# Kernel tuning notes

Measured on AMD Instinct MI355X. Metric: run time of the kernel, lower is better.

Reference implementation:

```python
import jax, jax.numpy as jnp
import numpy as np

N_NODES = 100000
N_EDGES = 600000
D_IN = 128
D_HID = 128


def gcn_conv(x, W, b, src, dst, n_nodes):
    # PyG GCNConv: add self-loops, symmetric deg^-1/2 normalization,
    # linear transform, scatter-add aggregation, bias.
    xw = x @ W  # [N, H]
    self_loop = jnp.arange(n_nodes, dtype=src.dtype)
    s = jnp.concatenate([src, self_loop])  # sources j
    d = jnp.concatenate([dst, self_loop])  # targets i
    deg = jax.ops.segment_sum(jnp.ones_like(d, dtype=xw.dtype), d,
                              num_segments=n_nodes)
    dinv = jnp.where(deg > 0, jax.lax.rsqrt(deg), 0.0)
    norm = dinv[s] * dinv[d]  # [E+N]
    msg = xw[s] * norm[:, None]  # gather + scale
    out = jax.ops.segment_sum(msg, d, num_segments=n_nodes)
    return out + b


def setup_inputs() -> dict:
    key = jax.random.key(0)
    ks = jax.random.split(key, 4)
    x = jax.random.normal(ks[0], (N_NODES, D_IN), dtype=jnp.float32)
    edge_index = jax.random.randint(ks[1], (2, N_EDGES), 0, N_NODES,
                                    dtype=jnp.int32)
    W1 = jax.random.normal(ks[2], (D_IN, D_HID), dtype=jnp.float32) / np.sqrt(D_IN)
    b1 = jnp.zeros((D_HID,), dtype=jnp.float32)
    W2 = jax.random.normal(ks[3], (D_HID, D_HID), dtype=jnp.float32) / np.sqrt(D_HID)
    b2 = jnp.zeros((D_HID,), dtype=jnp.float32)
    return {"x": x, "edge_index": edge_index, "W1": W1, "b1": b1,
            "W2": W2, "b2": b2}


def reference(x, edge_index, W1, b1, W2, b2):
    src, dst = edge_index[0], edge_index[1]
    n = x.shape[0]
    z = gcn_conv(x, W1, b1, src, dst, n)
    z = jax.nn.relu(z)
    z = gcn_conv(z, W2, b2, src, dst, n)
    # decode: per-edge dot product of endpoint embeddings
    return jnp.sum(z[src] * z[dst], axis=1)  # [E]
```

## Files before the change

### kernel.cpp

```cpp
#include <hip/hip_runtime.h>


typedef __attribute__((ext_vector_type(8))) short short8;
typedef __attribute__((ext_vector_type(4))) float f32x4;

__device__ __forceinline__ unsigned bf16_rne(float x) {
  unsigned u = __builtin_bit_cast(unsigned, x);
  return (u + 0x7FFFu + ((u >> 16) & 1u)) >> 16;
}
__device__ __forceinline__ float bf2f(unsigned short u) {
  return __builtin_bit_cast(float, ((unsigned)u) << 16);
}

__device__ __forceinline__ void wpack_body(const float* __restrict__ W,
                                           short* __restrict__ Wp, int t) {
  int lane = t & 63;
  int kf = (t >> 6) & 3;
  int ct = t >> 8;
  int col = ct * 16 + (lane & 15);
  int k0 = kf * 32 + (lane >> 4) * 8;
  short* dh = Wp + ((((0 * 8 + ct) * 4 + kf) * 64) + lane) * 8;
  short* dl = Wp + ((((1 * 8 + ct) * 4 + kf) * 64) + lane) * 8;
  for (int j = 0; j < 8; ++j) {
    float w = W[(k0 + j) * 128 + col];
    unsigned h = bf16_rne(w);
    float hf = __builtin_bit_cast(float, h << 16);
    unsigned lo = bf16_rne(w - hf);
    dh[j] = (short)h;
    dl[j] = (short)lo;
  }
}

__global__ __launch_bounds__(256) void prep_kernel(const float* __restrict__ W1,
                                                   short* __restrict__ Wp1,
                                                   const float* __restrict__ W2,
                                                   short* __restrict__ Wp2,
                                                   const int* __restrict__ dst,
                                                   int* __restrict__ deg,
                                                   int* __restrict__ slot, int E) {
  const int b = blockIdx.x;
  if (b < 8) {
    wpack_body(W1, Wp1, b * 256 + threadIdx.x);
  } else if (b < 16) {
    wpack_body(W2, Wp2, (b - 8) * 256 + threadIdx.x);
  } else {
    int base = (b - 16) * 1024 + threadIdx.x;
#pragma unroll
    for (int i = 0; i < 4; ++i) {
      int e = base + i * 256;
      if (e < E) slot[e] = atomicAdd(&deg[dst[e]], 1);
    }
  }
}

__global__ __launch_bounds__(512) void scan1_kernel(const int* __restrict__ in,
                                                    int* __restrict__ tmp,
                                                    int* __restrict__ bsums, int n) {
  __shared__ int sm[2][512];
  int t = threadIdx.x;
  int gid = blockIdx.x * 512 + t;
  int v = (gid < n) ? in[gid] : 0;
  int pp = 0;
  sm[0][t] = v;
  __syncthreads();
  for (int off = 1; off < 512; off <<= 1) {
    int nv = sm[pp][t];
    if (t >= off) nv += sm[pp][t - off];
    sm[pp ^ 1][t] = nv;
    pp ^= 1;
    __syncthreads();
  }
  int inc = sm[pp][t];
  if (gid < n) tmp[gid] = inc;
  if (t == 511) bsums[blockIdx.x] = inc;
}

__global__ __launch_bounds__(256) void scan23_kernel(const int* __restrict__ tmp,
                                                     const int* __restrict__ bsums,
                                                     const int* __restrict__ deg,
                                                     int* __restrict__ rowptr,
                                                     float* __restrict__ dinv,
                                                     int n, int nb) {
  __shared__ int sm[2][256];
  __shared__ int orig[256];
  int t = threadIdx.x;
  int v = (t < nb) ? bsums[t] : 0;
  orig[t] = v;
  int pp = 0;
  sm[0][t] = v;
  __syncthreads();
  for (int off = 1; off < 256; off <<= 1) {
    int nv = sm[pp][t];
    if (t >= off) nv += sm[pp][t - off];
    sm[pp ^ 1][t] = nv;
    pp ^= 1;
    __syncthreads();
  }
  int gid = blockIdx.x * 256 + t;
  if (gid < n) {
    int b = gid >> 9;
    rowptr[gid + 1] = tmp[gid] + (sm[pp][b] - orig[b]);
    dinv[gid] = rsqrtf((float)(deg[gid] + 1));
  }
  if (gid == 0) rowptr[0] = 0;
}

__global__ __launch_bounds__(256, 4) void scatgemm_kernel(
    const int* __restrict__ src, const int* __restrict__ dst,
    const int* __restrict__ rowptr, const int* __restrict__ slot,
    int2* __restrict__ csr, int E, int SCB, const float* __restrict__ A,
    const short* __restrict__ Wp, const float* __restrict__ dinv,
    unsigned short* __restrict__ out, int M) {
  __shared__ short8 lds_a[256];

  if ((int)blockIdx.x < SCB) {
    int base = blockIdx.x * 1024 + threadIdx.x;
#pragma unroll
    for (int i = 0; i < 4; ++i) {
      int e = base + i * 256;
      if (e < E) {
        int d = dst[e];
        csr[rowptr[d] + slot[e]] = make_int2(src[e], e);
      }
    }
    return;
  }

  const int bid = blockIdx.x - SCB;
  const int tid = threadIdx.x;
  const int wave = tid >> 6;
  const int lane = tid & 63;
  const int quad = lane >> 4;
  const int l15 = lane & 15;
  const int ct0 = wave * 2;
  const int ct1 = wave * 2 + 1;
  const int colbase = wave * 32 + l15;
  const int rb0 = bid * 16;
  const bool full = (rb0 + 16 <= M);
  const short8* Wp8 = (const short8*)Wp;

  {
    const int row = tid >> 4;
    const int seg = tid & 15;
    float4 a0 = {0.f, 0.f, 0.f, 0.f}, a1 = {0.f, 0.f, 0.f, 0.f};
    if (full || rb0 + row < M) {
      const float4* p = (const float4*)A + (size_t)(rb0 + row) * 32 + seg * 2;
      a0 = p[0];
      a1 = p[1];
    }
    const float av[8] = {a0.x, a0.y, a0.z, a0.w, a1.x, a1.y, a1.z, a1.w};
    short8 w;
#pragma unroll
    for (int j = 0; j < 8; ++j) w[j] = (short)bf16_rne(av[j]);
    lds_a[row * 16 + (seg ^ (row & 7))] = w;
  }

  short8 bh0[4], bh1[4], bl0[4], bl1[4];
#pragma unroll
  for (int f = 0; f < 4; ++f) {
    bh0[f] = Wp8[((0 * 8 + ct0) * 4 + f) * 64 + lane];
    bh1[f] = Wp8[((0 * 8 + ct1) * 4 + f) * 64 + lane];
    bl0[f] = Wp8[((1 * 8 + ct0) * 4 + f) * 64 + lane];
    bl1[f] = Wp8[((1 * 8 + ct1) * 4 + f) * 64 + lane];
  }

  __syncthreads();

  short8 af[4];
#pragma unroll
  for (int f = 0; f < 4; ++f) af[f] = lds_a[l15 * 16 + ((f * 4 + quad) ^ (l15 & 7))];

  f32x4 a0h = {0.f, 0.f, 0.f, 0.f};
  f32x4 a0l = {0.f, 0.f, 0.f, 0.f};
  f32x4 a1h = {0.f, 0.f, 0.f, 0.f};
  f32x4 a1l = {0.f, 0.f, 0.f, 0.f};
#pragma unroll
  for (int f = 0; f < 4; ++f) {
    a0h = __builtin_amdgcn_mfma_f32_16x16x32_bf16(af[f], bh0[f], a0h, 0, 0, 0);
    a1h = __builtin_amdgcn_mfma_f32_16x16x32_bf16(af[f], bh1[f], a1h, 0, 0, 0);
    a0l = __builtin_amdgcn_mfma_f32_16x16x32_bf16(af[f], bl0[f], a0l, 0, 0, 0);
    a1l = __builtin_amdgcn_mfma_f32_16x16x32_bf16(af[f], bl1[f], a1l, 0, 0, 0);
  }

  if (full) {
    const f32x4 dv = *(const f32x4*)(dinv + rb0 + quad * 4);
#pragma unroll
    for (int i = 0; i < 4; ++i) {
      const int r = rb0 + quad * 4 + i;
      out[(size_t)r * 128 + colbase] =
          (unsigned short)bf16_rne((a0h[i] + a0l[i]) * dv[i]);
      out[(size_t)r * 128 + colbase + 16] =
          (unsigned short)bf16_rne((a1h[i] + a1l[i]) * dv[i]);
    }
  } else {
#pragma unroll
    for (int i = 0; i < 4; ++i) {
      const int r = rb0 + quad * 4 + i;
      if (r < M) {
        const float d = dinv[r];
        out[(size_t)r * 128 + colbase] =
            (unsigned short)bf16_rne((a0h[i] + a0l[i]) * d);
        out[(size_t)r * 128 + colbase + 16] =
            (unsigned short)bf16_rne((a1h[i] + a1l[i]) * d);
      }
    }
  }
}

__global__ __launch_bounds__(256) void agg_gemm_kernel(
    const unsigned short* __restrict__ xw, const float* __restrict__ dinv,
    const int* __restrict__ rowptr, const int2* __restrict__ csr,
    const float* __restrict__ bias, const short* __restrict__ Wp,
    unsigned short* __restrict__ out, int N) {
  __shared__ short8 z1t[16][16];

  const int tid = threadIdx.x;
  const int node0 = blockIdx.x * 16;
  const int n = tid >> 4;
  const int l = tid & 15;
  const int node = node0 + n;

  short8 o = {0, 0, 0, 0, 0, 0, 0, 0};
  if (node < N) {
    const short8* xw8 = (const short8*)xw;
    short8 sv = xw8[(size_t)node * 16 + l];
    float acc[8];
#pragma unroll
    for (int j = 0; j < 8; ++j) acc[j] = bf2f((unsigned short)sv[j]);
    int s = rowptr[node], e = rowptr[node + 1];
    int k = s;
    for (; k + 4 <= e; k += 4) {
      int j0 = csr[k].x, j1 = csr[k + 1].x, j2 = csr[k + 2].x, j3 = csr[k + 3].x;
      short8 v0 = xw8[(size_t)j0 * 16 + l];
      short8 v1 = xw8[(size_t)j1 * 16 + l];
      short8 v2 = xw8[(size_t)j2 * 16 + l];
      short8 v3 = xw8[(size_t)j3 * 16 + l];
#pragma unroll
      for (int j = 0; j < 8; ++j) {
        acc[j] += (bf2f((unsigned short)v0[j]) + bf2f((unsigned short)v1[j])) +
                  (bf2f((unsigned short)v2[j]) + bf2f((unsigned short)v3[j]));
      }
    }
    for (; k < e; ++k) {
      short8 v = xw8[(size_t)csr[k].x * 16 + l];
#pragma unroll
      for (int j = 0; j < 8; ++j) acc[j] += bf2f((unsigned short)v[j]);
    }
    float di = dinv[node];
    const float4* b4 = (const float4*)bias;
    float4 bb0 = b4[l * 2], bb1 = b4[l * 2 + 1];
    float bv[8] = {bb0.x, bb0.y, bb0.z, bb0.w, bb1.x, bb1.y, bb1.z, bb1.w};
#pragma unroll
    for (int j = 0; j < 8; ++j) {
      float v = fmaf(di, acc[j], bv[j]);
      v = fmaxf(v, 0.f);
      o[j] = (short)bf16_rne(v);
    }
  }
  z1t[n][l ^ n] = o;
  __syncthreads();

  const int wave = tid >> 6;
  const int lane = tid & 63;
  const int quad = lane >> 4;
  const int l15 = lane & 15;
  const int ct0 = wave * 2;
  const int ct1 = wave * 2 + 1;

  short8 af[4];
#pragma unroll
  for (int f = 0; f < 4; ++f) af[f] = z1t[l15][(f * 4 + quad) ^ l15];

  const short8* Wp8 = (const short8*)Wp;
  f32x4 a0h = {0.f, 0.f, 0.f, 0.f};
  f32x4 a0l = {0.f, 0.f, 0.f, 0.f};
  f32x4 a1h = {0.f, 0.f, 0.f, 0.f};
  f32x4 a1l = {0.f, 0.f, 0.f, 0.f};
#pragma unroll
  for (int f = 0; f < 4; ++f) {
    const short8 bh0 = Wp8[((0 * 8 + ct0) * 4 + f) * 64 + lane];
    const short8 bh1 = Wp8[((0 * 8 + ct1) * 4 + f) * 64 + lane];
    const short8 bl0 = Wp8[((1 * 8 + ct0) * 4 + f) * 64 + lane];
    const short8 bl1 = Wp8[((1 * 8 + ct1) * 4 + f) * 64 + lane];
    a0h = __builtin_amdgcn_mfma_f32_16x16x32_bf16(af[f], bh0, a0h, 0, 0, 0);
    a1h = __builtin_amdgcn_mfma_f32_16x16x32_bf16(af[f], bh1, a1h, 0, 0, 0);
    a0l = __builtin_amdgcn_mfma_f32_16x16x32_bf16(af[f], bl0, a0l, 0, 0, 0);
    a1l = __builtin_amdgcn_mfma_f32_16x16x32_bf16(af[f], bl1, a1l, 0, 0, 0);
  }

  if (node0 + 16 <= N) {
    const f32x4 dv = *(const f32x4*)(dinv + node0 + quad * 4);
#pragma unroll
    for (int i = 0; i < 4; ++i) {
      const int r = node0 + quad * 4 + i;
      out[(size_t)r * 128 + ct0 * 16 + l15] =
          (unsigned short)bf16_rne((a0h[i] + a0l[i]) * dv[i]);
      out[(size_t)r * 128 + ct1 * 16 + l15] =
          (unsigned short)bf16_rne((a1h[i] + a1l[i]) * dv[i]);
    }
  } else {
#pragma unroll
    for (int i = 0; i < 4; ++i) {
      const int r = node0 + quad * 4 + i;
      if (r < N) {
        const float d = dinv[r];
        out[(size_t)r * 128 + ct0 * 16 + l15] =
            (unsigned short)bf16_rne((a0h[i] + a0l[i]) * d);
        out[(size_t)r * 128 + ct1 * 16 + l15] =
            (unsigned short)bf16_rne((a1h[i] + a1l[i]) * d);
      }
    }
  }
}

__global__ __launch_bounds__(128) void agg_kernel(const unsigned short* __restrict__ xw,
                                                  const float* __restrict__ dinv,
                                                  const int* __restrict__ rowptr,
                                                  const int2* __restrict__ csr,
                                                  const float* __restrict__ bias,
                                                  unsigned short* __restrict__ out,
                                                  int relu, int N) {
  int node = blockIdx.x * 8 + (threadIdx.x >> 4);
  int l = threadIdx.x & 15;
  if (node >= N) return;
  const short8* xw8 = (const short8*)xw;
  short8 sv = xw8[(size_t)node * 16 + l];
  float acc[8];
#pragma unroll
  for (int j = 0; j < 8; ++j) acc[j] = bf2f((unsigned short)sv[j]);
  int s = rowptr[node], e = rowptr[node + 1];
  int k = s;
  for (; k + 4 <= e; k += 4) {
    int j0 = csr[k].x, j1 = csr[k + 1].x, j2 = csr[k + 2].x, j3 = csr[k + 3].x;
    short8 v0 = xw8[(size_t)j0 * 16 + l];
    short8 v1 = xw8[(size_t)j1 * 16 + l];
    short8 v2 = xw8[(size_t)j2 * 16 + l];
    short8 v3 = xw8[(size_t)j3 * 16 + l];
#pragma unroll
    for (int j = 0; j < 8; ++j) {
      acc[j] += (bf2f((unsigned short)v0[j]) + bf2f((unsigned short)v1[j])) +
                (bf2f((unsigned short)v2[j]) + bf2f((unsigned short)v3[j]));
    }
  }
  for (; k < e; ++k) {
    short8 v = xw8[(size_t)csr[k].x * 16 + l];
#pragma unroll
    for (int j = 0; j < 8; ++j) acc[j] += bf2f((unsigned short)v[j]);
  }
  float di = dinv[node];
  const float4* b4 = (const float4*)bias;
  float4 bb0 = b4[l * 2], bb1 = b4[l * 2 + 1];
  float bv[8] = {bb0.x, bb0.y, bb0.z, bb0.w, bb1.x, bb1.y, bb1.z, bb1.w};
  short8 o;
#pragma unroll
  for (int j = 0; j < 8; ++j) {
    float v = fmaf(di, acc[j], bv[j]);
    if (relu) v = fmaxf(v, 0.f);
    o[j] = (short)bf16_rne(v);
  }
  ((short8*)out)[(size_t)node * 16 + l] = o;
}

__global__ __launch_bounds__(128) void decode_kernel(const unsigned short* __restrict__ z,
                                                     const int* __restrict__ rowptr,
                                                     const int2* __restrict__ csr,
                                                     float* __restrict__ out, int N) {
  int node = blockIdx.x * 8 + (threadIdx.x >> 4);
  int l = threadIdx.x & 15;
  if (node >= N) return;
  const short8* z8 = (const short8*)z;
  short8 zv = z8[(size_t)node * 16 + l];
  float zd[8];
#pragma unroll
  for (int j = 0; j < 8; ++j) zd[j] = bf2f((unsigned short)zv[j]);
  int s = rowptr[node], e = rowptr[node + 1];
  int k = s;
  for (; k + 4 <= e; k += 4) {
    int2 c0 = csr[k], c1 = csr[k + 1], c2 = csr[k + 2], c3 = csr[k + 3];
    short8 v0 = z8[(size_t)c0.x * 16 + l];
    short8 v1 = z8[(size_t)c1.x * 16 + l];
    short8 v2 = z8[(size_t)c2.x * 16 + l];
    short8 v3 = z8[(size_t)c3.x * 16 + l];
    float p0 = 0.f, p1 = 0.f, p2 = 0.f, p3 = 0.f;
#pragma unroll
    for (int j = 0; j < 8; ++j) {
      p0 = fmaf(zd[j], bf2f((unsigned short)v0[j]), p0);
      p1 = fmaf(zd[j], bf2f((unsigned short)v1[j]), p1);
      p2 = fmaf(zd[j], bf2f((unsigned short)v2[j]), p2);
      p3 = fmaf(zd[j], bf2f((unsigned short)v3[j]), p3);
    }
#pragma unroll
    for (int off = 8; off > 0; off >>= 1) {
      p0 += __shfl_xor(p0, off);
      p1 += __shfl_xor(p1, off);
      p2 += __shfl_xor(p2, off);
      p3 += __shfl_xor(p3, off);
    }
    if (l == 0) {
      out[c0.y] = p0;
      out[c1.y] = p1;
      out[c2.y] = p2;
      out[c3.y] = p3;
    }
  }
  for (; k < e; ++k) {
    int2 c = csr[k];
    short8 v = z8[(size_t)c.x * 16 + l];
    float p = 0.f;
#pragma unroll
    for (int j = 0; j < 8; ++j) p = fmaf(zd[j], bf2f((unsigned short)v[j]), p);
#pragma unroll
    for (int off = 8; off > 0; off >>= 1) p += __shfl_xor(p, off);
    if (l == 0) out[c.y] = p;
  }
}

extern "C" void kernel_launch(void* const* d_in, const int* in_sizes, int n_in,
                              void* d_out, int out_size, void* d_ws, size_t ws_size,
                              hipStream_t stream) {
  const float* x  = (const float*)d_in[0];
  const int*   ei = (const int*)d_in[1];
  const float* W1 = (const float*)d_in[2];
  const float* b1 = (const float*)d_in[3];
  const float* W2 = (const float*)d_in[4];
  const float* b2 = (const float*)d_in[5];

  const int N = in_sizes[0] / 128;
  const int E = in_sizes[1] / 2;
  const int* src = ei;
  const int* dst = ei + E;

  char* ws = (char*)d_ws;
  size_t off = 0;
  auto alloc = [&](size_t bytes) -> void* {
    void* p = ws + off;
    off += (bytes + 255) & ~(size_t)255;
    return p;
  };
  unsigned short* bufA = (unsigned short*)alloc((size_t)N * 128 * 2);
  unsigned short* bufB = (unsigned short*)alloc((size_t)N * 128 * 2);
  float* dinv    = (float*)alloc((size_t)N * 4);
  int*   rowptr  = (int*)alloc((size_t)(N + 1) * 4);
  int2*  csr     = (int2*)alloc((size_t)E * 8);
  short* Wp1     = (short*)alloc((size_t)2 * 8 * 4 * 64 * 8 * 2);
  short* Wp2     = (short*)alloc((size_t)2 * 8 * 4 * 64 * 8 * 2);
  int*   tmp     = (int*)alloc((size_t)N * 4);
  int*   slot    = (int*)alloc((size_t)E * 4);
  int*   deg     = (int*)alloc((size_t)N * 4);
  int*   bsums   = (int*)alloc(1024);
  size_t zbytes = ((char*)bsums + 1024) - (char*)deg;
  hipMemsetAsync(deg, 0, zbytes, stream);

  const int E4B = (E + 1023) / 1024;
  const int NB = (N + 255) / 256;
  const int SB = (N + 511) / 512;
  const int G16 = (N + 15) / 16;
  const int AB16 = (N + 15) / 16;
  const int AB8 = (N + 7) / 8;

  prep_kernel<<<16 + E4B, 256, 0, stream>>>(W1, Wp1, W2, Wp2, dst, deg, slot, E);
  scan1_kernel<<<SB, 512, 0, stream>>>(deg, tmp, bsums, N);
  scan23_kernel<<<NB, 256, 0, stream>>>(tmp, bsums, deg, rowptr, dinv, N, SB);
  scatgemm_kernel<<<E4B + G16, 256, 0, stream>>>(src, dst, rowptr, slot, csr, E,
                                                 E4B, x, Wp1, dinv, bufA, N);
  agg_gemm_kernel<<<AB16, 256, 0, stream>>>(bufA, dinv, rowptr, csr, b1, Wp2,
                                            bufB, N);
  agg_kernel<<<AB8, 128, 0, stream>>>(bufB, dinv, rowptr, csr, b2, bufA, 0, N);
  decode_kernel<<<AB8, 128, 0, stream>>>(bufA, rowptr, csr, (float*)d_out, N);
}
```

Before: 259.6 us.

## Prefetch next CSR index batch in gather loops and shrink agg/decode blocks

Software-pipelines the neighbor loops in agg_gemm, agg and decode so the next four CSR entries load while the current four feature rows are gathered, hiding index-load latency. It also halves the agg and decode block size to 64 threads (one wavefront, 4 nodes per block), and doubles the edges per block in the degree-counting part of prep. The prefetch costs extra registers and may lower occupancy, and smaller blocks mean more blocks to schedule.

```diff
diff --git a/kernel.cpp b/kernel.cpp
--- a/kernel.cpp
+++ b/kernel.cpp
@@ -44,9 +44,9 @@
   } else if (b < 16) {
     wpack_body(W2, Wp2, (b - 8) * 256 + threadIdx.x);
   } else {
-    int base = (b - 16) * 1024 + threadIdx.x;
-#pragma unroll
-    for (int i = 0; i < 4; ++i) {
+    int base = (b - 16) * 2048 + threadIdx.x;
+#pragma unroll
+    for (int i = 0; i < 8; ++i) {
       int e = base + i * 256;
       if (e < E) slot[e] = atomicAdd(&deg[dst[e]], 1);
     }
@@ -229,17 +229,24 @@
     for (int j = 0; j < 8; ++j) acc[j] = bf2f((unsigned short)sv[j]);
     int s = rowptr[node], e = rowptr[node + 1];
     int k = s;
-    for (; k + 4 <= e; k += 4) {
-      int j0 = csr[k].x, j1 = csr[k + 1].x, j2 = csr[k + 2].x, j3 = csr[k + 3].x;
-      short8 v0 = xw8[(size_t)j0 * 16 + l];
-      short8 v1 = xw8[(size_t)j1 * 16 + l];
-      short8 v2 = xw8[(size_t)j2 * 16 + l];
-      short8 v3 = xw8[(size_t)j3 * 16 + l];
+    int2 c0 = {0, 0}, c1 = {0, 0}, c2 = {0, 0}, c3 = {0, 0};
+    bool have = (k + 4 <= e);
+    if (have) { c0 = csr[k]; c1 = csr[k + 1]; c2 = csr[k + 2]; c3 = csr[k + 3]; }
+    while (have) {
+      const int kn = k + 4;
+      const bool hn = (kn + 4 <= e);
+      int2 n0 = {0, 0}, n1 = {0, 0}, n2 = {0, 0}, n3 = {0, 0};
+      if (hn) { n0 = csr[kn]; n1 = csr[kn + 1]; n2 = csr[kn + 2]; n3 = csr[kn + 3]; }
+      short8 v0 = xw8[(size_t)c0.x * 16 + l];
+      short8 v1 = xw8[(size_t)c1.x * 16 + l];
+      short8 v2 = xw8[(size_t)c2.x * 16 + l];
+      short8 v3 = xw8[(size_t)c3.x * 16 + l];
 #pragma unroll
       for (int j = 0; j < 8; ++j) {
         acc[j] += (bf2f((unsigned short)v0[j]) + bf2f((unsigned short)v1[j])) +
                   (bf2f((unsigned short)v2[j]) + bf2f((unsigned short)v3[j]));
       }
+      k = kn; have = hn; c0 = n0; c1 = n1; c2 = n2; c3 = n3;
     }
     for (; k < e; ++k) {
       short8 v = xw8[(size_t)csr[k].x * 16 + l];
@@ -313,14 +320,14 @@
   }
 }
 
-__global__ __launch_bounds__(128) void agg_kernel(const unsigned short* __restrict__ xw,
-                                                  const float* __restrict__ dinv,
-                                                  const int* __restrict__ rowptr,
-                                                  const int2* __restrict__ csr,
-                                                  const float* __restrict__ bias,
-                                                  unsigned short* __restrict__ out,
-                                                  int relu, int N) {
-  int node = blockIdx.x * 8 + (threadIdx.x >> 4);
+__global__ __launch_bounds__(64) void agg_kernel(const unsigned short* __restrict__ xw,
+                                                 const float* __restrict__ dinv,
+                                                 const int* __restrict__ rowptr,
+                                                 const int2* __restrict__ csr,
+                                                 const float* __restrict__ bias,
+                                                 unsigned short* __restrict__ out,
+                                                 int relu, int N) {
+  int node = blockIdx.x * 4 + (threadIdx.x >> 4);
   int l = threadIdx.x & 15;
   if (node >= N) return;
   const short8* xw8 = (const short8*)xw;
@@ -330,17 +337,24 @@
   for (int j = 0; j < 8; ++j) acc[j] = bf2f((unsigned short)sv[j]);
   int s = rowptr[node], e = rowptr[node + 1];
   int k = s;
-  for (; k + 4 <= e; k += 4) {
-    int j0 = csr[k].x, j1 = csr[k + 1].x, j2 = csr[k + 2].x, j3 = csr[k + 3].x;
-    short8 v0 = xw8[(size_t)j0 * 16 + l];
-    short8 v1 = xw8[(size_t)j1 * 16 + l];
-    short8 v2 = xw8[(size_t)j2 * 16 + l];
-    short8 v3 = xw8[(size_t)j3 * 16 + l];
+  int2 c0 = {0, 0}, c1 = {0, 0}, c2 = {0, 0}, c3 = {0, 0};
+  bool have = (k + 4 <= e);
+  if (have) { c0 = csr[k]; c1 = csr[k + 1]; c2 = csr[k + 2]; c3 = csr[k + 3]; }
+  while (have) {
+    const int kn = k + 4;
+    const bool hn = (kn + 4 <= e);
+    int2 n0 = {0, 0}, n1 = {0, 0}, n2 = {0, 0}, n3 = {0, 0};
+    if (hn) { n0 = csr[kn]; n1 = csr[kn + 1]; n2 = csr[kn + 2]; n3 = csr[kn + 3]; }
+    short8 v0 = xw8[(size_t)c0.x * 16 + l];
+    short8 v1 = xw8[(size_t)c1.x * 16 + l];
+    short8 v2 = xw8[(size_t)c2.x * 16 + l];
+    short8 v3 = xw8[(size_t)c3.x * 16 + l];
 #pragma unroll
     for (int j = 0; j < 8; ++j) {
       acc[j] += (bf2f((unsigned short)v0[j]) + bf2f((unsigned short)v1[j])) +
                 (bf2f((unsigned short)v2[j]) + bf2f((unsigned short)v3[j]));
     }
+    k = kn; have = hn; c0 = n0; c1 = n1; c2 = n2; c3 = n3;
   }
   for (; k < e; ++k) {
     short8 v = xw8[(size_t)csr[k].x * 16 + l];
@@ -361,11 +375,11 @@
   ((short8*)out)[(size_t)node * 16 + l] = o;
 }
 
-__global__ __launch_bounds__(128) void decode_kernel(const unsigned short* __restrict__ z,
-                                                     const int* __restrict__ rowptr,
-                                                     const int2* __restrict__ csr,
-                                                     float* __restrict__ out, int N) {
-  int node = blockIdx.x * 8 + (threadIdx.x >> 4);
+__global__ __launch_bounds__(64) void decode_kernel(const unsigned short* __restrict__ z,
+                                                    const int* __restrict__ rowptr,
+                                                    const int2* __restrict__ csr,
+                                                    float* __restrict__ out, int N) {
+  int node = blockIdx.x * 4 + (threadIdx.x >> 4);
   int l = threadIdx.x & 15;
   if (node >= N) return;
   const short8* z8 = (const short8*)z;
@@ -375,8 +389,14 @@
   for (int j = 0; j < 8; ++j) zd[j] = bf2f((unsigned short)zv[j]);
   int s = rowptr[node], e = rowptr[node + 1];
   int k = s;
-  for (; k + 4 <= e; k += 4) {
-    int2 c0 = csr[k], c1 = csr[k + 1], c2 = csr[k + 2], c3 = csr[k + 3];
+  int2 c0 = {0, 0}, c1 = {0, 0}, c2 = {0, 0}, c3 = {0, 0};
+  bool have = (k + 4 <= e);
+  if (have) { c0 = csr[k]; c1 = csr[k + 1]; c2 = csr[k + 2]; c3 = csr[k + 3]; }
+  while (have) {
+    const int kn = k + 4;
+    const bool hn = (kn + 4 <= e);
+    int2 n0 = {0, 0}, n1 = {0, 0}, n2 = {0, 0}, n3 = {0, 0};
+    if (hn) { n0 = csr[kn]; n1 = csr[kn + 1]; n2 = csr[kn + 2]; n3 = csr[kn + 3]; }
     short8 v0 = z8[(size_t)c0.x * 16 + l];
     short8 v1 = z8[(size_t)c1.x * 16 + l];
     short8 v2 = z8[(size_t)c2.x * 16 + l];
@@ -402,6 +422,7 @@
       out[c2.y] = p2;
       out[c3.y] = p3;
     }
+    k = kn; have = hn; c0 = n0; c1 = n1; c2 = n2; c3 = n3;
   }
   for (; k < e; ++k) {
     int2 c = csr[k];
@@ -452,19 +473,20 @@
   hipMemsetAsync(deg, 0, zbytes, stream);
 
   const int E4B = (E + 1023) / 1024;
+  const int E8B = (E + 2047) / 2048;
   const int NB = (N + 255) / 256;
   const int SB = (N + 511) / 512;
   const int G16 = (N + 15) / 16;
   const int AB16 = (N + 15) / 16;
-  const int AB8 = (N + 7) / 8;
-
-  prep_kernel<<<16 + E4B, 256, 0, stream>>>(W1, Wp1, W2, Wp2, dst, deg, slot, E);
+  const int AB4 = (N + 3) / 4;
+
+  prep_kernel<<<16 + E8B, 256, 0, stream>>>(W1, Wp1, W2, Wp2, dst, deg, slot, E);
   scan1_kernel<<<SB, 512, 0, stream>>>(deg, tmp, bsums, N);
   scan23_kernel<<<NB, 256, 0, stream>>>(tmp, bsums, deg, rowptr, dinv, N, SB);
   scatgemm_kernel<<<E4B + G16, 256, 0, stream>>>(src, dst, rowptr, slot, csr, E,
                                                  E4B, x, Wp1, dinv, bufA, N);
   agg_gemm_kernel<<<AB16, 256, 0, stream>>>(bufA, dinv, rowptr, csr, b1, Wp2,
                                             bufB, N);
-  agg_kernel<<<AB8, 128, 0, stream>>>(bufB, dinv, rowptr, csr, b2, bufA, 0, N);
-  decode_kernel<<<AB8, 128, 0, stream>>>(bufA, rowptr, csr, (float*)d_out, N);
-}
+  agg_kernel<<<AB4, 64, 0, stream>>>(bufB, dinv, rowptr, csr, b2, bufA, 0, N);
+  decode_kernel<<<AB4, 64, 0, stream>>>(bufA, rowptr, csr, (float*)d_out, N);
+}
```

Result: no change. 260.5 us (+0.3%).
